# Kernel tuning notes

Measured on AMD Instinct MI355X. Metric: run time of the kernel, lower is better.

## Reference

```python
import jax, jax.numpy as jnp
import numpy as np

B, S, D = 16, 2048, 1024  # batch, max_len, inp_size == hidden_size


def setup_inputs() -> dict:
    key = jax.random.key(0)
    k1, k2, k3, k4, k5, k6 = jax.random.split(key, 6)
    stdv = 1.0 / np.sqrt(D)
    return {
        "encoder_outputs": jax.random.normal(k1, (B, S, D), dtype=jnp.float32),
        "hidden": jax.random.normal(k2, (B, D), dtype=jnp.float32),
        "lengths": jax.random.randint(k3, (B,), 1, S + 1, dtype=jnp.int32),
        "W": jax.random.normal(k4, (D, 2 * D), dtype=jnp.float32) * stdv,
        "b": jax.random.normal(k5, (D,), dtype=jnp.float32) * stdv,
        "v": jax.random.normal(k6, (D,), dtype=jnp.float32) * stdv,
    }


def reference(encoder_outputs, hidden, lengths, W, b, v):
    # Linear on cat([H, enc]) == H @ Wh^T + enc @ We^T + b (avoids materializing the concat)
    Wh, We = W[:, :D], W[:, D:]              # [D_out, D] each
    hid_proj = hidden @ Wh.T                  # [B, D]
    enc_proj = jnp.einsum('bsd,ed->bse', encoder_outputs, We)  # [B, S, D]
    energy = jnp.tanh(enc_proj + hid_proj[:, None, :] + b)     # [B, S, D]
    scores = jnp.einsum('bsd,d->bs', energy, v)                # [B, S]
    # mask positions >= length to -inf before softmax
    valid = jnp.arange(S)[None, :] < lengths[:, None]          # [B, S]
    scores = jnp.where(valid, scores, -jnp.inf)
    attn = jax.nn.softmax(scores, axis=-1)                     # [B, S]
    context = jnp.einsum('bs,bsd->bd', attn, encoder_outputs)  # [B, D]
    return context[:, None, :]                                 # [B, 1, D] to match torch bmm output
```

## Files before the change

### kernel.cpp

```cpp
#include <hip/hip_runtime.h>
#include <cstdint>

#define DEV static __device__ __forceinline__

typedef __attribute__((__ext_vector_type__(8))) __bf16 bf16x8;
typedef __attribute__((__ext_vector_type__(4))) float f32x4;

static constexpr int Bc = 16, Sc = 2048, Dc = 1024;

DEV unsigned short f2bf(float x) {
  unsigned int u = __float_as_uint(x);
  unsigned int r = (u + 0x7fffu + ((u >> 16) & 1u)) >> 16;
  return (unsigned short)r;
}
DEV unsigned int pack2(float a, float b) {
  return (unsigned int)f2bf(a) | ((unsigned int)f2bf(b) << 16);
}
DEV float tanh_fast(float x) {
  return 1.f - 2.f / (__expf(2.f * x) + 1.f);
}
DEV void gload16(const void* g, void* l) {
  __builtin_amdgcn_global_load_lds(
      (const __attribute__((address_space(1))) unsigned int*)g,
      (__attribute__((address_space(3))) unsigned int*)l, 16, 0, 0);
}

__global__ __launch_bounds__(256) void k_prep(const float* __restrict__ enc,
                                              const float* __restrict__ hidden,
                                              const float* __restrict__ W,
                                              const float* __restrict__ bias,
                                              const int* __restrict__ lengths,
                                              unsigned short* __restrict__ ebf,
                                              unsigned short* __restrict__ webf,
                                              float* __restrict__ hp,
                                              int* __restrict__ wl) {
  int bx = blockIdx.x;
  int t = threadIdx.x;
  if (bx < 2048) {
    int team = t >> 7, lane = t & 127;
    int r0 = bx * 16;
    int b = r0 >> 11;
    int len = lengths[b];
    for (int rr = team; rr < 16; rr += 2) {
      int s = (r0 + rr) & 2047;
      if (s >= len) continue;
      const float* src = enc + (size_t)(r0 + rr) * Dc + lane * 8;
      unsigned short* dst = ebf + (size_t)(r0 + rr) * Dc + lane * 8;
      float4 f0 = *(const float4*)src;
      float4 f1 = *(const float4*)(src + 4);
      uint4 o;
      o.x = pack2(f0.x, f0.y);
      o.y = pack2(f0.z, f0.w);
      o.z = pack2(f1.x, f1.y);
      o.w = pack2(f1.z, f1.w);
      *(uint4*)dst = o;
    }
  } else if (bx < 3072) {
    int e = bx - 2048;
    if (e == 0) {
      int sblk = t >> 4, b = t & 15;
      int active = (sblk * 128 < lengths[b]) ? 1 : 0;
      unsigned long long mask = __ballot(active);
      int lane = t & 63, wid = t >> 6;
      int prefix = __popcll(mask & ((1ull << lane) - 1ull));
      __shared__ int woff[4];
      if (lane == 0) woff[wid] = __popcll(mask);
      __syncthreads();
      int base = 0;
      for (int i = 0; i < wid; i++) base += woff[i];
      if (active) wl[1 + base + prefix] = (b << 8) | sblk;
      if (t == 0) wl[0] = woff[0] + woff[1] + woff[2] + woff[3];
    }
    __shared__ float wrow[Dc];
    for (int i = t; i < Dc; i += 256) wrow[i] = W[(size_t)e * 2048 + i];
    __syncthreads();
    int w = t >> 6, lane = t & 63;
    float bv = bias[e];
    for (int bi = w; bi < Bc; bi += 4) {
      float s = 0.f;
      const float* hrow = hidden + (size_t)bi * Dc;
      for (int d = lane; d < Dc; d += 64) s += hrow[d] * wrow[d];
      for (int m = 1; m < 64; m <<= 1) s += __shfl_xor(s, m);
      if (lane == 0) hp[(size_t)bi * Dc + e] = s + bv;
    }
  } else {
    int i = ((bx - 3072) * 256 + t) * 8;
    int e = i >> 10, d = i & 1023;
    const float* p = W + (size_t)e * 2048 + 1024 + d;
    float4 f0 = *(const float4*)p;
    float4 f1 = *(const float4*)(p + 4);
    uint4 o;
    o.x = pack2(f0.x, f0.y);
    o.y = pack2(f0.z, f0.w);
    o.z = pack2(f1.x, f1.y);
    o.w = pack2(f1.z, f1.w);
    *(uint4*)(webf + i) = o;
  }
}

__global__ __launch_bounds__(256) void k_scores(const unsigned short* __restrict__ Ae,
                                                const unsigned short* __restrict__ We,
                                                const float* __restrict__ hp,
                                                const float* __restrict__ v,
                                                const int* __restrict__ wl,
                                                float* __restrict__ pscores) {
  int g = blockIdx.x & 255;
  int et = blockIdx.x >> 8;
  if (g >= wl[0]) return;
  int pk = wl[1 + g];
  int b = pk >> 8, sblk = pk & 255;
  int s0 = sblk * 128;
  int m0 = b * Sc + s0;
  int e0 = et * 128;

  __shared__ unsigned short As0[128 * 32];
  __shared__ unsigned short As1[128 * 32];
  __shared__ unsigned short Bs0[128 * 32];
  __shared__ unsigned short Bs1[128 * 32];
  float* sc_s = (float*)As0;

  int t = threadIdx.x;
  int w = t >> 6, lane = t & 63;

  f32x4 acc[4][4] = {};
  int wr = w >> 1, wc = w & 1;

  {
    int o = t >> 3, q = t & 7;
    int g8 = q ^ (o & 7);
    int srow = 2 * o + (g8 >> 2);
    int scol = (g8 & 3) * 8;
    Ae += (size_t)(m0 + srow) * Dc + scol;
    We += (size_t)(e0 + srow) * Dc + scol;
  }
  const unsigned short* ga0 = Ae;
  const unsigned short* gb0 = We;

  int posw = (((lane & 1) << 2) + (lane >> 4)) ^ (((lane & 15) >> 1) & 7);
  int aoff = (wr * 32 + ((lane & 15) >> 1)) * 64 + posw * 8;
  int boff = (wc * 32 + ((lane & 15) >> 1)) * 64 + posw * 8;

  auto stage = [&](int k0, unsigned short* A, unsigned short* B) {
    gload16(ga0 + k0, A + w * 512);
    gload16(ga0 + k0 + 64 * Dc, A + 2048 + w * 512);
    gload16(gb0 + k0, B + w * 512);
    gload16(gb0 + k0 + 64 * Dc, B + 2048 + w * 512);
  };
  auto compute = [&](const unsigned short* A, const unsigned short* B) {
    bf16x8 af[4], bfr[4];
#pragma unroll
    for (int m = 0; m < 4; m++)
      af[m] = __builtin_bit_cast(bf16x8, *(const uint4*)(A + aoff + m * 512));
#pragma unroll
    for (int n = 0; n < 4; n++)
      bfr[n] = __builtin_bit_cast(bf16x8, *(const uint4*)(B + boff + n * 512));
    __builtin_amdgcn_s_setprio(1);
#pragma unroll
    for (int m = 0; m < 4; m++)
#pragma unroll
      for (int n = 0; n < 4; n++)
        acc[m][n] = __builtin_amdgcn_mfma_f32_16x16x32_bf16(af[m], bfr[n], acc[m][n], 0, 0, 0);
    __builtin_amdgcn_s_setprio(0);
  };

  stage(0, As0, Bs0);

#pragma unroll 1
  for (int i2 = 0; i2 < 15; ++i2) {
    stage((2 * i2 + 1) * 32, As1, Bs1);
    asm volatile("s_waitcnt vmcnt(4)" ::: "memory");
    __builtin_amdgcn_sched_barrier(0);
    __builtin_amdgcn_s_barrier();
    __builtin_amdgcn_sched_barrier(0);
    compute(As0, Bs0);
    __builtin_amdgcn_sched_barrier(0);
    __builtin_amdgcn_s_barrier();
    stage((2 * i2 + 2) * 32, As0, Bs0);
    asm volatile("s_waitcnt vmcnt(4)" ::: "memory");
    __builtin_amdgcn_sched_barrier(0);
    __builtin_amdgcn_s_barrier();
    __builtin_amdgcn_sched_barrier(0);
    compute(As1, Bs1);
    __builtin_amdgcn_sched_barrier(0);
    __builtin_amdgcn_s_barrier();
  }
  stage(31 * 32, As1, Bs1);
  asm volatile("s_waitcnt vmcnt(4)" ::: "memory");
  __builtin_amdgcn_sched_barrier(0);
  __builtin_amdgcn_s_barrier();
  __builtin_amdgcn_sched_barrier(0);
  compute(As0, Bs0);
  __builtin_amdgcn_sched_barrier(0);
  __builtin_amdgcn_s_barrier();
  asm volatile("s_waitcnt vmcnt(0)" ::: "memory");
  __builtin_amdgcn_sched_barrier(0);
  __builtin_amdgcn_s_barrier();
  __builtin_amdgcn_sched_barrier(0);
  compute(As1, Bs1);

  float hpv[4], vv[4];
#pragma unroll
  for (int n = 0; n < 4; n++) {
    int ec = wc * 64 + n * 16 + (lane & 15);
    hpv[n] = hp[(size_t)b * Dc + e0 + ec];
    vv[n] = v[e0 + ec];
  }
  if (t < 128) sc_s[t] = 0.f;
  __syncthreads();

  for (int m = 0; m < 4; m++) {
    float rs0 = 0.f, rs1 = 0.f, rs2 = 0.f, rs3 = 0.f;
#pragma unroll
    for (int n = 0; n < 4; n++) {
      f32x4 a = acc[m][n];
      rs0 += vv[n] * tanh_fast(a[0] + hpv[n]);
      rs1 += vv[n] * tanh_fast(a[1] + hpv[n]);
      rs2 += vv[n] * tanh_fast(a[2] + hpv[n]);
      rs3 += vv[n] * tanh_fast(a[3] + hpv[n]);
    }
    for (int mask = 1; mask < 16; mask <<= 1) {
      rs0 += __shfl_xor(rs0, mask);
      rs1 += __shfl_xor(rs1, mask);
      rs2 += __shfl_xor(rs2, mask);
      rs3 += __shfl_xor(rs3, mask);
    }
    if ((lane & 15) == 0) {
      int rbase = wr * 64 + m * 16 + (lane >> 4) * 4;
      atomicAdd(&sc_s[rbase + 0], rs0);
      atomicAdd(&sc_s[rbase + 1], rs1);
      atomicAdd(&sc_s[rbase + 2], rs2);
      atomicAdd(&sc_s[rbase + 3], rs3);
    }
  }
  __syncthreads();
  if (t < 128) pscores[((size_t)et * Bc + b) * Sc + s0 + t] = sc_s[t];
}

__global__ __launch_bounds__(256) void k_softmax(const float* __restrict__ pscores,
                                                 const int* __restrict__ lengths,
                                                 float* __restrict__ attn) {
  int b = blockIdx.x, t = threadIdx.x;
  int len = lengths[b];
  float vals[8];
  float mx = -INFINITY;
  for (int i = 0; i < 8; i++) {
    int s = t + i * 256;
    float sc = 0.f;
    for (int p = 0; p < 8; p++) sc += pscores[((size_t)p * Bc + b) * Sc + s];
    sc = (s < len) ? sc : -INFINITY;
    vals[i] = sc;
    mx = fmaxf(mx, sc);
  }
  for (int m = 1; m < 64; m <<= 1) mx = fmaxf(mx, __shfl_xor(mx, m));
  __shared__ float rmax[4], rsum[4];
  int w = t >> 6, lane = t & 63;
  if (lane == 0) rmax[w] = mx;
  __syncthreads();
  mx = fmaxf(fmaxf(rmax[0], rmax[1]), fmaxf(rmax[2], rmax[3]));
  float sm = 0.f;
  for (int i = 0; i < 8; i++) {
    vals[i] = __expf(vals[i] - mx);
    sm += vals[i];
  }
  for (int m = 1; m < 64; m <<= 1) sm += __shfl_xor(sm, m);
  if (lane == 0) rsum[w] = sm;
  __syncthreads();
  sm = rsum[0] + rsum[1] + rsum[2] + rsum[3];
  float inv = 1.f / sm;
  for (int i = 0; i < 8; i++) attn[(size_t)b * Sc + t + i * 256] = vals[i] * inv;
}

__global__ __launch_bounds__(256) void k_ctx(const unsigned short* __restrict__ ebf,
                                             const float* __restrict__ attn,
                                             const int* __restrict__ lengths,
                                             float* __restrict__ pctx) {
  int b = blockIdx.x >> 6, sp = blockIdx.x & 63;
  int t = threadIdx.x;
  int d0 = t * 4;
  int sbeg = sp * 32;
  float* outp = pctx + ((size_t)sp * Bc + b) * Dc + d0;
  int len = lengths[b];
  if (sbeg >= len) {
    *(float4*)outp = make_float4(0.f, 0.f, 0.f, 0.f);
    return;
  }
  __shared__ float at_s[32];
  if (t < 32) at_s[t] = attn[(size_t)b * Sc + sbeg + t];
  __syncthreads();
  float4 a = make_float4(0.f, 0.f, 0.f, 0.f);
  const unsigned short* ebase = ebf + ((size_t)b * Sc + sbeg) * Dc + d0;
  int ns = min(32, len - sbeg);
  for (int i = 0; i < ns; i++) {
    float wt = at_s[i];
    uint2 u = *(const uint2*)(ebase + (size_t)i * Dc);
    a.x += wt * __uint_as_float(u.x << 16);
    a.y += wt * __uint_as_float(u.x & 0xffff0000u);
    a.z += wt * __uint_as_float(u.y << 16);
    a.w += wt * __uint_as_float(u.y & 0xffff0000u);
  }
  *(float4*)outp = a;
}

__global__ __launch_bounds__(256) void k_reduce(const float* __restrict__ pctx,
                                               float* __restrict__ out) {
  int i = blockIdx.x * 256 + threadIdx.x;
  int b = i >> 10, d = i & 1023;
  float s = 0.f;
  for (int p = 0; p < 64; p++) s += pctx[((size_t)p * Bc + b) * Dc + d];
  out[i] = s;
}

extern "C" void kernel_launch(void* const* d_in, const int* in_sizes, int n_in,
                              void* d_out, int out_size, void* d_ws, size_t ws_size,
                              hipStream_t stream) {
  const float* enc = (const float*)d_in[0];
  const float* hidden = (const float*)d_in[1];
  const int* lengths = (const int*)d_in[2];
  const float* W = (const float*)d_in[3];
  const float* bias = (const float*)d_in[4];
  const float* v = (const float*)d_in[5];
  float* out = (float*)d_out;

  char* ws = (char*)d_ws;
  unsigned short* ebf = (unsigned short*)ws;
  unsigned short* webf = (unsigned short*)(ws + 67108864);
  float* hp = (float*)(ws + 69206016);
  float* pscores = (float*)(ws + 69271552);
  float* attn = (float*)(ws + 70320128);
  float* pctx = (float*)(ws + 70451200);
  int* wl = (int*)(ws + 74645504);

  hipLaunchKernelGGL(k_prep, dim3(3584), dim3(256), 0, stream, enc, hidden, W, bias,
                     lengths, ebf, webf, hp, wl);
  hipLaunchKernelGGL(k_scores, dim3(2048), dim3(256), 0, stream, ebf, webf, hp, v,
                     wl, pscores);
  hipLaunchKernelGGL(k_softmax, dim3(16), dim3(256), 0, stream, pscores, lengths, attn);
  hipLaunchKernelGGL(k_ctx, dim3(1024), dim3(256), 0, stream, ebf, attn, lengths, pctx);
  hipLaunchKernelGGL(k_reduce, dim3(64), dim3(256), 0, stream, pctx, out);
}
```

Before: 95.94 us.

## Use single-wave 64x64 score tiles without barriers and coarsen context split

The scores GEMM changes from 256-thread blocks computing 128x128 tiles to 64-thread single-wave blocks computing 64x64 tiles. This removes all workgroup barriers and the shared-memory atomic score reduction. The price is less data reuse per loaded tile and twice as many partial-score slices (16 instead of 8) for softmax to sum. The context kernel also processes 128 sequence positions per block instead of 32, which leaves fewer partial context rows for the final reduce but means fewer blocks.

```diff
diff --git a/kernel.cpp b/kernel.cpp
--- a/kernel.cpp
+++ b/kernel.cpp
@@ -98,36 +98,33 @@
   }
 }
 
-__global__ __launch_bounds__(256) void k_scores(const unsigned short* __restrict__ Ae,
-                                                const unsigned short* __restrict__ We,
-                                                const float* __restrict__ hp,
-                                                const float* __restrict__ v,
-                                                const int* __restrict__ wl,
-                                                float* __restrict__ pscores) {
+__global__ __launch_bounds__(64) void k_scores(const unsigned short* __restrict__ Ae,
+                                               const unsigned short* __restrict__ We,
+                                               const float* __restrict__ hp,
+                                               const float* __restrict__ v,
+                                               const int* __restrict__ wl,
+                                               float* __restrict__ pscores) {
   int g = blockIdx.x & 255;
-  int et = blockIdx.x >> 8;
+  int tile = blockIdx.x >> 8;
   if (g >= wl[0]) return;
+  int et = tile & 15, mt = tile >> 4;
   int pk = wl[1 + g];
   int b = pk >> 8, sblk = pk & 255;
   int s0 = sblk * 128;
-  int m0 = b * Sc + s0;
-  int e0 = et * 128;
-
-  __shared__ unsigned short As0[128 * 32];
-  __shared__ unsigned short As1[128 * 32];
-  __shared__ unsigned short Bs0[128 * 32];
-  __shared__ unsigned short Bs1[128 * 32];
-  float* sc_s = (float*)As0;
-
-  int t = threadIdx.x;
-  int w = t >> 6, lane = t & 63;
-
+  int m0 = b * Sc + s0 + mt * 64;
+  int e0 = et * 64;
+
+  __shared__ unsigned short As0[64 * 32];
+  __shared__ unsigned short As1[64 * 32];
+  __shared__ unsigned short Bs0[64 * 32];
+  __shared__ unsigned short Bs1[64 * 32];
+
+  int lane = threadIdx.x;
   f32x4 acc[4][4] = {};
-  int wr = w >> 1, wc = w & 1;
 
   {
-    int o = t >> 3, q = t & 7;
-    int g8 = q ^ (o & 7);
+    int o = lane >> 3, q = lane & 7;
+    int g8 = q ^ o;
     int srow = 2 * o + (g8 >> 2);
     int scol = (g8 & 3) * 8;
     Ae += (size_t)(m0 + srow) * Dc + scol;
@@ -137,14 +134,14 @@
   const unsigned short* gb0 = We;
 
   int posw = (((lane & 1) << 2) + (lane >> 4)) ^ (((lane & 15) >> 1) & 7);
-  int aoff = (wr * 32 + ((lane & 15) >> 1)) * 64 + posw * 8;
-  int boff = (wc * 32 + ((lane & 15) >> 1)) * 64 + posw * 8;
+  int aoff = ((lane & 15) >> 1) * 64 + posw * 8;
 
   auto stage = [&](int k0, unsigned short* A, unsigned short* B) {
-    gload16(ga0 + k0, A + w * 512);
-    gload16(ga0 + k0 + 64 * Dc, A + 2048 + w * 512);
-    gload16(gb0 + k0, B + w * 512);
-    gload16(gb0 + k0 + 64 * Dc, B + 2048 + w * 512);
+#pragma unroll
+    for (int c = 0; c < 4; c++) {
+      gload16(ga0 + k0 + c * 16 * Dc, A + c * 512);
+      gload16(gb0 + k0 + c * 16 * Dc, B + c * 512);
+    }
   };
   auto compute = [&](const unsigned short* A, const unsigned short* B) {
     bf16x8 af[4], bfr[4];
@@ -153,7 +150,7 @@
       af[m] = __builtin_bit_cast(bf16x8, *(const uint4*)(A + aoff + m * 512));
 #pragma unroll
     for (int n = 0; n < 4; n++)
-      bfr[n] = __builtin_bit_cast(bf16x8, *(const uint4*)(B + boff + n * 512));
+      bfr[n] = __builtin_bit_cast(bf16x8, *(const uint4*)(B + aoff + n * 512));
     __builtin_amdgcn_s_setprio(1);
 #pragma unroll
     for (int m = 0; m < 4; m++)
@@ -168,46 +165,33 @@
 #pragma unroll 1
   for (int i2 = 0; i2 < 15; ++i2) {
     stage((2 * i2 + 1) * 32, As1, Bs1);
-    asm volatile("s_waitcnt vmcnt(4)" ::: "memory");
-    __builtin_amdgcn_sched_barrier(0);
-    __builtin_amdgcn_s_barrier();
+    asm volatile("s_waitcnt vmcnt(8)" ::: "memory");
     __builtin_amdgcn_sched_barrier(0);
     compute(As0, Bs0);
     __builtin_amdgcn_sched_barrier(0);
-    __builtin_amdgcn_s_barrier();
     stage((2 * i2 + 2) * 32, As0, Bs0);
-    asm volatile("s_waitcnt vmcnt(4)" ::: "memory");
-    __builtin_amdgcn_sched_barrier(0);
-    __builtin_amdgcn_s_barrier();
+    asm volatile("s_waitcnt vmcnt(8)" ::: "memory");
     __builtin_amdgcn_sched_barrier(0);
     compute(As1, Bs1);
     __builtin_amdgcn_sched_barrier(0);
-    __builtin_amdgcn_s_barrier();
   }
   stage(31 * 32, As1, Bs1);
-  asm volatile("s_waitcnt vmcnt(4)" ::: "memory");
-  __builtin_amdgcn_sched_barrier(0);
-  __builtin_amdgcn_s_barrier();
+  asm volatile("s_waitcnt vmcnt(8)" ::: "memory");
   __builtin_amdgcn_sched_barrier(0);
   compute(As0, Bs0);
   __builtin_amdgcn_sched_barrier(0);
-  __builtin_amdgcn_s_barrier();
   asm volatile("s_waitcnt vmcnt(0)" ::: "memory");
   __builtin_amdgcn_sched_barrier(0);
-  __builtin_amdgcn_s_barrier();
-  __builtin_amdgcn_sched_barrier(0);
   compute(As1, Bs1);
 
   float hpv[4], vv[4];
 #pragma unroll
   for (int n = 0; n < 4; n++) {
-    int ec = wc * 64 + n * 16 + (lane & 15);
-    hpv[n] = hp[(size_t)b * Dc + e0 + ec];
-    vv[n] = v[e0 + ec];
-  }
-  if (t < 128) sc_s[t] = 0.f;
-  __syncthreads();
-
+    int ec = e0 + n * 16 + (lane & 15);
+    hpv[n] = hp[(size_t)b * Dc + ec];
+    vv[n] = v[ec];
+  }
+  float* outp = pscores + ((size_t)et * Bc + b) * Sc + s0 + mt * 64;
   for (int m = 0; m < 4; m++) {
     float rs0 = 0.f, rs1 = 0.f, rs2 = 0.f, rs3 = 0.f;
 #pragma unroll
@@ -225,15 +209,13 @@
       rs3 += __shfl_xor(rs3, mask);
     }
     if ((lane & 15) == 0) {
-      int rbase = wr * 64 + m * 16 + (lane >> 4) * 4;
-      atomicAdd(&sc_s[rbase + 0], rs0);
-      atomicAdd(&sc_s[rbase + 1], rs1);
-      atomicAdd(&sc_s[rbase + 2], rs2);
-      atomicAdd(&sc_s[rbase + 3], rs3);
-    }
-  }
-  __syncthreads();
-  if (t < 128) pscores[((size_t)et * Bc + b) * Sc + s0 + t] = sc_s[t];
+      int r = m * 16 + (lane >> 4) * 4;
+      outp[r + 0] = rs0;
+      outp[r + 1] = rs1;
+      outp[r + 2] = rs2;
+      outp[r + 3] = rs3;
+    }
+  }
 }
 
 __global__ __launch_bounds__(256) void k_softmax(const float* __restrict__ pscores,
@@ -246,7 +228,7 @@
   for (int i = 0; i < 8; i++) {
     int s = t + i * 256;
     float sc = 0.f;
-    for (int p = 0; p < 8; p++) sc += pscores[((size_t)p * Bc + b) * Sc + s];
+    for (int p = 0; p < 16; p++) sc += pscores[((size_t)p * Bc + b) * Sc + s];
     sc = (s < len) ? sc : -INFINITY;
     vals[i] = sc;
     mx = fmaxf(mx, sc);
@@ -274,22 +256,22 @@
                                              const float* __restrict__ attn,
                                              const int* __restrict__ lengths,
                                              float* __restrict__ pctx) {
-  int b = blockIdx.x >> 6, sp = blockIdx.x & 63;
+  int b = blockIdx.x >> 4, sp = blockIdx.x & 15;
   int t = threadIdx.x;
   int d0 = t * 4;
-  int sbeg = sp * 32;
+  int sbeg = sp * 128;
   float* outp = pctx + ((size_t)sp * Bc + b) * Dc + d0;
   int len = lengths[b];
   if (sbeg >= len) {
     *(float4*)outp = make_float4(0.f, 0.f, 0.f, 0.f);
     return;
   }
-  __shared__ float at_s[32];
-  if (t < 32) at_s[t] = attn[(size_t)b * Sc + sbeg + t];
+  __shared__ float at_s[128];
+  if (t < 128) at_s[t] = attn[(size_t)b * Sc + sbeg + t];
   __syncthreads();
   float4 a = make_float4(0.f, 0.f, 0.f, 0.f);
   const unsigned short* ebase = ebf + ((size_t)b * Sc + sbeg) * Dc + d0;
-  int ns = min(32, len - sbeg);
+  int ns = min(128, len - sbeg);
   for (int i = 0; i < ns; i++) {
     float wt = at_s[i];
     uint2 u = *(const uint2*)(ebase + (size_t)i * Dc);
@@ -306,7 +288,7 @@
   int i = blockIdx.x * 256 + threadIdx.x;
   int b = i >> 10, d = i & 1023;
   float s = 0.f;
-  for (int p = 0; p < 64; p++) s += pctx[((size_t)p * Bc + b) * Dc + d];
+  for (int p = 0; p < 16; p++) s += pctx[((size_t)p * Bc + b) * Dc + d];
   out[i] = s;
 }
 
@@ -326,15 +308,15 @@
   unsigned short* webf = (unsigned short*)(ws + 67108864);
   float* hp = (float*)(ws + 69206016);
   float* pscores = (float*)(ws + 69271552);
-  float* attn = (float*)(ws + 70320128);
-  float* pctx = (float*)(ws + 70451200);
-  int* wl = (int*)(ws + 74645504);
+  float* attn = (float*)(ws + 71368704);
+  float* pctx = (float*)(ws + 71499776);
+  int* wl = (int*)(ws + 72548352);
 
   hipLaunchKernelGGL(k_prep, dim3(3584), dim3(256), 0, stream, enc, hidden, W, bias,
                      lengths, ebf, webf, hp, wl);
-  hipLaunchKernelGGL(k_scores, dim3(2048), dim3(256), 0, stream, ebf, webf, hp, v,
+  hipLaunchKernelGGL(k_scores, dim3(8192), dim3(64), 0, stream, ebf, webf, hp, v,
                      wl, pscores);
   hipLaunchKernelGGL(k_softmax, dim3(16), dim3(256), 0, stream, pscores, lengths, attn);
-  hipLaunchKernelGGL(k_ctx, dim3(1024), dim3(256), 0, stream, ebf, attn, lengths, pctx);
+  hipLaunchKernelGGL(k_ctx, dim3(256), dim3(256), 0, stream, ebf, attn, lengths, pctx);
   hipLaunchKernelGGL(k_reduce, dim3(64), dim3(256), 0, stream, pctx, out);
 }
```

Measured after the change: 118.0 us. +23.0%, slower.
